# Kernel tuning notes

Measured on AMD Instinct MI355X. Metric: run time of the kernel, lower is better.

The kernel has to match this reference:

```python
import jax, jax.numpy as jnp
import numpy as np

VOCAB_SIZE = 148
START_IDX = 1
LATENT = 32
HID = 256
NUM_LAYERS = 2
B = 8192
T = 50


def setup_inputs() -> dict:
    key = jax.random.key(0)
    ks = jax.random.split(key, 20)
    s = 0.05
    inp = {
        "z": jax.random.normal(ks[0], (B, LATENT), jnp.float32),
        "target_tokens": jax.random.randint(ks[1], (B, T), 0, VOCAB_SIZE),
        "emb": jax.random.normal(ks[2], (VOCAB_SIZE, HID), jnp.float32) * s,
        "W_lat": jax.random.normal(ks[3], (HID * NUM_LAYERS, LATENT), jnp.float32) * s,
        "b_lat": jnp.zeros((HID * NUM_LAYERS,), jnp.float32),
        "W_ih0": jax.random.normal(ks[4], (3 * HID, HID), jnp.float32) * s,
        "W_hh0": jax.random.normal(ks[5], (3 * HID, HID), jnp.float32) * s,
        "b_ih0": jnp.zeros((3 * HID,), jnp.float32),
        "b_hh0": jnp.zeros((3 * HID,), jnp.float32),
        "W_ih1": jax.random.normal(ks[6], (3 * HID, HID), jnp.float32) * s,
        "W_hh1": jax.random.normal(ks[7], (3 * HID, HID), jnp.float32) * s,
        "b_ih1": jnp.zeros((3 * HID,), jnp.float32),
        "b_hh1": jnp.zeros((3 * HID,), jnp.float32),
        "W1": jax.random.normal(ks[8], (HID, HID), jnp.float32) * s,
        "b1": jnp.zeros((HID,), jnp.float32),
        "W2": jax.random.normal(ks[9], (VOCAB_SIZE, HID), jnp.float32) * s,
        "b2": jnp.zeros((VOCAB_SIZE,), jnp.float32),
    }
    # padding_idx=0 row of embedding is zero in torch
    inp["emb"] = inp["emb"].at[0].set(0.0)
    return inp


def _gru_cell(x, h, W_ih, W_hh, b_ih, b_hh):
    # PyTorch GRUCell math
    gi = x @ W_ih.T + b_ih          # [B, 3H]
    gh = h @ W_hh.T + b_hh          # [B, 3H]
    i_r, i_z, i_n = jnp.split(gi, 3, axis=-1)
    h_r, h_z, h_n = jnp.split(gh, 3, axis=-1)
    r = jax.nn.sigmoid(i_r + h_r)
    zg = jax.nn.sigmoid(i_z + h_z)
    n = jnp.tanh(i_n + r * h_n)
    return (1.0 - zg) * n + zg * h


def reference(z, target_tokens, emb, W_lat, b_lat,
              W_ih0, W_hh0, b_ih0, b_hh0,
              W_ih1, W_hh1, b_ih1, b_hh1,
              W1, b1, W2, b2):
    batch = z.shape[0]
    # init hidden: (B, L*H) -> (L, B, H)
    h = (z @ W_lat.T + b_lat).reshape(batch, NUM_LAYERS, HID).transpose(1, 0, 2)
    # teacher forcing ratio 1.0: inputs = [START, tgt[:,1], ..., tgt[:,T-2]]
    start = jnp.full((batch, 1), START_IDX, dtype=target_tokens.dtype)
    tokens_in = jnp.concatenate([start, target_tokens[:, 1:T - 1]], axis=1)  # [B, T-1]
    x = emb[tokens_in]                       # [B, T-1, H]
    xs = x.transpose(1, 0, 2)                # [T-1, B, H]

    def step(carry, x_t):
        h0, h1 = carry
        h0n = _gru_cell(x_t, h0, W_ih0, W_hh0, b_ih0, b_hh0)
        h1n = _gru_cell(h0n, h1, W_ih1, W_hh1, b_ih1, b_hh1)
        return (h0n, h1n), h1n

    _, ys = jax.lax.scan(step, (h[0], h[1]), xs)   # ys: [T-1, B, H]
    y = ys.transpose(1, 0, 2)                      # [B, T-1, H]
    hdd = jax.nn.relu(jnp.einsum('bth,oh->bto', y, W1) + b1)
    logits = jnp.einsum('bth,vh->btv', hdd, W2) + b2   # [B, T-1, V]
    generated = target_tokens[:, 1:]                   # pure teacher forcing
    return logits, generated
```

## Files before the change

### kernel.cpp

```cpp
#include <hip/hip_runtime.h>
#include <hip/hip_bf16.h>
#include <math.h>


#define BATCH 8192
#define TTOT 50
#define TS 49
#define HID 256
#define N3 768
#define VOCAB 148
#define START_TOK 1
#define HPAD 264

typedef short bf16x8 __attribute__((ext_vector_type(8)));
typedef float f32x4 __attribute__((ext_vector_type(4)));

constexpr size_t OFF_Y    = 0;
constexpr size_t OFF_WH0B = OFF_Y + 205520896;
constexpr size_t OFF_WI1B = OFF_WH0B + 393216;
constexpr size_t OFF_WH1B = OFF_WI1B + 393216;
constexpr size_t OFF_W1B  = OFF_WH1B + 393216;
constexpr size_t OFF_W2B  = OFF_W1B + 131072;
constexpr size_t OFF_TAB  = OFF_W2B + 81920;
constexpr size_t OFF_TABN = OFF_TAB + 303104;
constexpr size_t OFF_H0F  = OFF_TAB + 454656;
constexpr size_t OFF_H1F  = OFF_H0F + 8388608;

__device__ __forceinline__ short f2b(float f) {
    union { float f; unsigned int u; } v; v.f = f;
    unsigned int u = v.u;
    return (short)((u + 0x7FFFu + ((u >> 16) & 1u)) >> 16);
}
__device__ __forceinline__ float sigm(float x) {
    return 1.f / (1.f + __expf(-x));
}
__device__ __forceinline__ float tanh_(float x) {
    x = fmaxf(x, -15.f);
    float e = __expf(-2.f * x);
    return (1.f - e) / (1.f + e);
}

__global__ __launch_bounds__(256) void convert_w(
    const float* __restrict__ Wh0, const float* __restrict__ Wi1, const float* __restrict__ Wh1,
    const float* __restrict__ W1, const float* __restrict__ W2,
    short* __restrict__ Wh0b, short* __restrict__ Wi1b, short* __restrict__ Wh1b,
    short* __restrict__ W1b, short* __restrict__ W2b)
{
    int tid = blockIdx.x * 256 + threadIdx.x;
    const int WSZ = N3 * HID;
    const float* S; short* D; int n; bool pad148 = false;
    if (tid < WSZ) { S = Wh0; D = Wh0b; n = tid; }
    else if (tid < 2 * WSZ) { S = Wi1; D = Wi1b; n = tid - WSZ; }
    else if (tid < 3 * WSZ) { S = Wh1; D = Wh1b; n = tid - 2 * WSZ; }
    else if (tid < 3 * WSZ + 65536) { S = W1; D = W1b; n = tid - 3 * WSZ; }
    else if (tid < 3 * WSZ + 65536 + 40960) { S = W2; D = W2b; n = tid - 3 * WSZ - 65536; pad148 = true; }
    else return;
    int e = n & 7, lane = (n >> 3) & 63, kc = (n >> 9) & 7, nt = n >> 12;
    int row = nt * 16 + (lane & 15);
    int k = kc * 32 + (lane >> 4) * 8 + e;
    float v = (pad148 && row >= VOCAB) ? 0.f : S[row * HID + k];
    D[n] = f2b(v);
}

__global__ __launch_bounds__(256) void build_tab2(
    const float* __restrict__ emb, const float* __restrict__ Wih0,
    const float* __restrict__ bih0, const float* __restrict__ bhh0,
    float* __restrict__ tab_rz, float* __restrict__ tab_n)
{
    int o = blockIdx.x * 256 + threadIdx.x;
    if (o >= VOCAB * N3) return;
    int v = o / N3, cc = o - v * N3;
    int g = cc >> 8, c = cc & 255;
    const float* er = emb + v * HID;
    const float* wr = Wih0 + cc * HID;
    float s = bih0[cc];
    #pragma unroll 8
    for (int k = 0; k < HID; ++k) s += er[k] * wr[k];
    if (g == 0)      tab_rz[(((v << 8) + c) << 1) + 0] = s + bhh0[c];
    else if (g == 1) tab_rz[(((v << 8) + c) << 1) + 1] = s + bhh0[256 + c];
    else             tab_n[(v << 8) + c] = s;
}

__global__ __launch_bounds__(256) void init_h(
    const float* __restrict__ z, const float* __restrict__ Wl, const float* __restrict__ bl,
    float* __restrict__ h0f, float* __restrict__ h1f)
{
    int tid = blockIdx.x * 256 + threadIdx.x;
    int b = tid >> 9, o = tid & 511;
    const float* zr = z + b * 32;
    const float* wr = Wl + o * 32;
    float s = bl[o];
    #pragma unroll
    for (int k = 0; k < 32; ++k) s += zr[k] * wr[k];
    if (o < HID) h0f[b * HID + o] = s;
    else         h1f[b * HID + o - HID] = s;
}

__global__ __launch_bounds__(512) __attribute__((amdgpu_waves_per_eu(4)))
void gru_persistent(
    const int* __restrict__ toks,
    const float* __restrict__ tab_rz, const float* __restrict__ tab_n,
    const short* __restrict__ Wh0, const short* __restrict__ Wi1, const short* __restrict__ Wh1,
    const float* __restrict__ bhh0, const float* __restrict__ bih1, const float* __restrict__ bhh1,
    const float* __restrict__ h0f, const float* __restrict__ h1f,
    short* __restrict__ Yb)
{
    __shared__ short h0L[2][16 * HPAD];
    __shared__ short h1L[2][16 * HPAD];
    __shared__ int tokL[16 * TTOT];

    const int tid = threadIdx.x;
    const int wave = tid >> 6, lane = tid & 63, quad = lane >> 4, l15 = lane & 15;
    const int rowbase = blockIdx.x * 16;

    {
        int row = tid >> 5, col = (tid & 31) * 8;
        const float* s0 = h0f + (size_t)(rowbase + row) * HID + col;
        const float* s1 = h1f + (size_t)(rowbase + row) * HID + col;
        short t0[8], t1[8];
        #pragma unroll
        for (int j = 0; j < 8; ++j) { t0[j] = f2b(s0[j]); t1[j] = f2b(s1[j]); }
        *(bf16x8*)&h0L[0][row * HPAD + col] = *(bf16x8*)t0;
        *(bf16x8*)&h1L[0][row * HPAD + col] = *(bf16x8*)t1;
    }
    for (int idx = tid; idx < 16 * TTOT; idx += 512) {
        int row = idx / TTOT, tt = idx - row * TTOT;
        tokL[idx] = (tt == 0) ? START_TOK : toks[(size_t)(rowbase + row) * TTOT + tt];
    }

    int colc[2]; colc[0] = wave * 32 + l15; colc[1] = colc[0] + 16;
    float h0r[2][4], h1r[2][4];
    #pragma unroll
    for (int c = 0; c < 2; ++c)
        #pragma unroll
        for (int r_ = 0; r_ < 4; ++r_) {
            int row = rowbase + quad * 4 + r_;
            h0r[c][r_] = h0f[(size_t)row * HID + colc[c]];
            h1r[c][r_] = h1f[(size_t)row * HID + colc[c]];
        }

    float bn0[2], brr[2], brz[2], bni[2], bnh[2];
    #pragma unroll
    for (int c = 0; c < 2; ++c) {
        int col = colc[c];
        bn0[c] = bhh0[512 + col];
        brr[c] = bih1[col] + bhh1[col];
        brz[c] = bih1[256 + col] + bhh1[256 + col];
        bni[c] = bih1[512 + col];
        bnh[c] = bhh1[512 + col];
    }

    int woff[6];
    #pragma unroll
    for (int g = 0; g < 3; ++g)
        #pragma unroll
        for (int c = 0; c < 2; ++c)
            woff[g * 2 + c] = ((g * 16 + wave * 2 + c) << 12) + lane * 8;

    const int a0base = l15 * HPAD + quad * 8;
    const int hwbase = (quad * 4) * HPAD + colc[0];
    int tokrow[4];
    #pragma unroll
    for (int r_ = 0; r_ < 4; ++r_) tokrow[r_] = (quad * 4 + r_) * TTOT;
    short* yptr = Yb + ((((size_t)blockIdx.x << 3) + wave) << 9) + lane * 8;

    int rb = 0, wb = 1;
    __syncthreads();

    for (int t = 0; t < TS; ++t) {
        f32x4 acc0[6] = {};
        #pragma unroll 1
        for (int kc = 0; kc < 8; ++kc) {
            bf16x8 a0 = *(const bf16x8*)&h0L[rb][a0base + kc * 32];
            #pragma unroll
            for (int j = 0; j < 6; ++j) {
                bf16x8 b0 = *(const bf16x8*)(Wh0 + woff[j] + kc * 512);
                acc0[j] = __builtin_amdgcn_mfma_f32_16x16x32_bf16(a0, b0, acc0[j], 0, 0, 0);
            }
        }
        #pragma unroll
        for (int r_ = 0; r_ < 4; ++r_) {
            int tok = tokL[tokrow[r_] + t];
            const float2 rz0 = *(const float2*)(tab_rz + (tok << 9) + (colc[0] << 1));
            const float2 rz1 = *(const float2*)(tab_rz + (tok << 9) + (colc[1] << 1));
            float in0 = tab_n[(tok << 8) + colc[0]];
            float in1 = tab_n[(tok << 8) + colc[1]];
            {
                float r = sigm(acc0[0][r_] + rz0.x);
                float z = sigm(acc0[2][r_] + rz0.y);
                float n = tanh_(in0 + r * (acc0[4][r_] + bn0[0]));
                h0r[0][r_] = n + z * (h0r[0][r_] - n);
            }
            {
                float r = sigm(acc0[1][r_] + rz1.x);
                float z = sigm(acc0[3][r_] + rz1.y);
                float n = tanh_(in1 + r * (acc0[5][r_] + bn0[1]));
                h0r[1][r_] = n + z * (h0r[1][r_] - n);
            }
        }
        #pragma unroll
        for (int r_ = 0; r_ < 4; ++r_) {
            unsigned u;
            asm("v_cvt_pk_bf16_f32 %0, %1, %2" : "=v"(u) : "v"(h0r[0][r_]), "v"(h0r[1][r_]));
            int ro = hwbase + r_ * HPAD;
            h0L[wb][ro]      = (short)u;
            h0L[wb][ro + 16] = (short)(u >> 16);
        }
        __syncthreads();

        f32x4 accrz[4] = {}, acchn[2] = {}, accgn[2] = {};
        #pragma unroll 1
        for (int kc = 0; kc < 8; ++kc) {
            bf16x8 a1 = *(const bf16x8*)&h1L[rb][a0base + kc * 32];
            bf16x8 an = *(const bf16x8*)&h0L[wb][a0base + kc * 32];
            #pragma unroll
            for (int j = 0; j < 6; ++j) {
                bf16x8 b1 = *(const bf16x8*)(Wh1 + woff[j] + kc * 512);
                if (j < 4) accrz[j] = __builtin_amdgcn_mfma_f32_16x16x32_bf16(a1, b1, accrz[j], 0, 0, 0);
                else       acchn[j - 4] = __builtin_amdgcn_mfma_f32_16x16x32_bf16(a1, b1, acchn[j - 4], 0, 0, 0);
            }
            #pragma unroll
            for (int j = 0; j < 6; ++j) {
                bf16x8 b = *(const bf16x8*)(Wi1 + woff[j] + kc * 512);
                if (j < 4) accrz[j] = __builtin_amdgcn_mfma_f32_16x16x32_bf16(an, b, accrz[j], 0, 0, 0);
                else       accgn[j - 4] = __builtin_amdgcn_mfma_f32_16x16x32_bf16(an, b, accgn[j - 4], 0, 0, 0);
            }
        }
        #pragma unroll
        for (int c = 0; c < 2; ++c)
            #pragma unroll
            for (int r_ = 0; r_ < 4; ++r_) {
                float r = sigm(accrz[c][r_] + brr[c]);
                float z = sigm(accrz[2 + c][r_] + brz[c]);
                float n = tanh_(accgn[c][r_] + bni[c] + r * (acchn[c][r_] + bnh[c]));
                h1r[c][r_] = n + z * (h1r[c][r_] - n);
            }
        #pragma unroll
        for (int r_ = 0; r_ < 4; ++r_) {
            unsigned u;
            asm("v_cvt_pk_bf16_f32 %0, %1, %2" : "=v"(u) : "v"(h1r[0][r_]), "v"(h1r[1][r_]));
            int ro = hwbase + r_ * HPAD;
            h1L[wb][ro]      = (short)u;
            h1L[wb][ro + 16] = (short)(u >> 16);
        }
        __syncthreads();

        *(bf16x8*)yptr = *(const bf16x8*)&h1L[wb][a0base + wave * 32];
        yptr += (size_t)512 * 8 * 512;

        rb ^= 1; wb ^= 1;
    }
}

__global__ __launch_bounds__(256) void head_kernel(
    const short* __restrict__ YP, const short* __restrict__ W1P, const float* __restrict__ b1,
    const short* __restrict__ W2P, const float* __restrict__ b2, float* __restrict__ out)
{
    __shared__ short hddL[64 * HPAD];
    int wave = threadIdx.x >> 6;
    int lane = threadIdx.x & 63;
    int quad = lane >> 4;
    int l15  = lane & 15;
    int rbase = blockIdx.x * 64;
    int tt = rbase >> 13;
    int mb = (rbase & 8191) >> 4;

    {
        const short* ybase = YP + ((size_t)tt * 512 + mb) * 4096 + lane * 8;
        const short* wbase = W1P + (size_t)(wave * 4) * 4096 + lane * 8;
        f32x4 acc[4][4] = {};
        #pragma unroll 2
        for (int kc = 0; kc < 8; ++kc) {
            bf16x8 a[4], bfr[4];
            #pragma unroll
            for (int i = 0; i < 4; ++i) a[i] = *(const bf16x8*)(ybase + (size_t)i * 4096 + kc * 512);
            #pragma unroll
            for (int j = 0; j < 4; ++j) bfr[j] = *(const bf16x8*)(wbase + (size_t)j * 4096 + kc * 512);
            #pragma unroll
            for (int i = 0; i < 4; ++i)
                #pragma unroll
                for (int j = 0; j < 4; ++j)
                    acc[i][j] = __builtin_amdgcn_mfma_f32_16x16x32_bf16(a[i], bfr[j], acc[i][j], 0, 0, 0);
        }
        #pragma unroll
        for (int i = 0; i < 4; ++i)
            #pragma unroll
            for (int j = 0; j < 4; ++j)
                #pragma unroll
                for (int r = 0; r < 4; ++r) {
                    int rl = i * 16 + quad * 4 + r;
                    int c  = wave * 64 + j * 16 + l15;
                    float v = acc[i][j][r] + b1[c];
                    hddL[rl * HPAD + c] = f2b(fmaxf(v, 0.f));
                }
    }
    __syncthreads();
    for (int s = wave * 5; s < wave * 5 + 5; ++s) {
        int ct = s >> 1, rh = s & 1;
        const short* w2b = W2P + (size_t)ct * 4096 + lane * 8;
        f32x4 acc2[2] = {};
        #pragma unroll 2
        for (int kc = 0; kc < 8; ++kc) {
            bf16x8 bfr = *(const bf16x8*)(w2b + kc * 512);
            #pragma unroll
            for (int it = 0; it < 2; ++it) {
                bf16x8 a = *(const bf16x8*)&hddL[(rh * 32 + it * 16 + l15) * HPAD + kc * 32 + quad * 8];
                acc2[it] = __builtin_amdgcn_mfma_f32_16x16x32_bf16(a, bfr, acc2[it], 0, 0, 0);
            }
        }
        int col = ct * 16 + l15;
        if (col < VOCAB) {
            #pragma unroll
            for (int it = 0; it < 2; ++it)
                #pragma unroll
                for (int r = 0; r < 4; ++r) {
                    int rl = rh * 32 + it * 16 + quad * 4 + r;
                    int gr = rbase + rl;
                    int t2 = gr >> 13;
                    int bb = gr & 8191;
                    out[((size_t)bb * TS + t2) * VOCAB + col] = acc2[it][r] + b2[col];
                }
        }
    }
}

__global__ __launch_bounds__(256) void gen_copy(const int* __restrict__ toks, float* __restrict__ out2)
{
    int tid = blockIdx.x * 256 + threadIdx.x;
    if (tid < BATCH * TS) {
        int b = tid / TS, j = tid - b * TS;
        out2[tid] = (float)toks[b * TTOT + j + 1];
    }
}

extern "C" void kernel_launch(void* const* d_in, const int* in_sizes, int n_in,
                              void* d_out, int out_size, void* d_ws, size_t ws_size,
                              hipStream_t stream) {
    const float* z     = (const float*)d_in[0];
    const int*   toks  = (const int*)d_in[1];
    const float* emb   = (const float*)d_in[2];
    const float* W_lat = (const float*)d_in[3];
    const float* b_lat = (const float*)d_in[4];
    const float* W_ih0 = (const float*)d_in[5];
    const float* W_hh0 = (const float*)d_in[6];
    const float* b_ih0 = (const float*)d_in[7];
    const float* b_hh0 = (const float*)d_in[8];
    const float* W_ih1 = (const float*)d_in[9];
    const float* W_hh1 = (const float*)d_in[10];
    const float* b_ih1 = (const float*)d_in[11];
    const float* b_hh1 = (const float*)d_in[12];
    const float* W1    = (const float*)d_in[13];
    const float* b1    = (const float*)d_in[14];
    const float* W2    = (const float*)d_in[15];
    const float* b2    = (const float*)d_in[16];

    char* w = (char*)d_ws;
    short* Yb    = (short*)(w + OFF_Y);
    short* Wh0b  = (short*)(w + OFF_WH0B);
    short* Wi1b  = (short*)(w + OFF_WI1B);
    short* Wh1b  = (short*)(w + OFF_WH1B);
    short* W1b   = (short*)(w + OFF_W1B);
    short* W2b   = (short*)(w + OFF_W2B);
    float* tabrz = (float*)(w + OFF_TAB);
    float* tabn  = (float*)(w + OFF_TABN);
    float* h0f   = (float*)(w + OFF_H0F);
    float* h1f   = (float*)(w + OFF_H1F);

    float* out_logits = (float*)d_out;
    float* out_gen    = out_logits + (size_t)BATCH * TS * VOCAB;

    convert_w<<<2720, 256, 0, stream>>>(W_hh0, W_ih1, W_hh1, W1, W2,
                                        Wh0b, Wi1b, Wh1b, W1b, W2b);
    build_tab2<<<(VOCAB * N3 + 255) / 256, 256, 0, stream>>>(emb, W_ih0, b_ih0, b_hh0, tabrz, tabn);
    init_h<<<(BATCH * 512) / 256, 256, 0, stream>>>(z, W_lat, b_lat, h0f, h1f);
    gen_copy<<<(BATCH * TS + 255) / 256, 256, 0, stream>>>(toks, out_gen);

    gru_persistent<<<512, 512, 0, stream>>>(toks, tabrz, tabn, Wh0b, Wi1b, Wh1b,
                                            b_hh0, b_ih1, b_hh1, h0f, h1f, Yb);

    head_kernel<<<(BATCH * TS) / 64, 256, 0, stream>>>(Yb, W1b, b1, W2b, b2, out_logits);
}
```

Baseline: 1.723 ms.

## Retile GRU kernel to 32 rows per block with 16 waves, reusing weight loads

The persistent GRU kernel now handles 32 batch rows per block using 1024 threads. Each wave owns 16 hidden columns for two 16-row M tiles instead of 32 columns for one tile, so every weight fragment loaded from global memory feeds two MFMAs. This is meant to halve per-block weight traffic and the grid is halved to 256 blocks. In exchange each CU gets fewer blocks and there are more waves per barrier, and the 1024-thread launch bound combined with waves_per_eu(4) may constrain register allocation.

```diff
diff --git a/kernel.cpp b/kernel.cpp
--- a/kernel.cpp
+++ b/kernel.cpp
@@ -96,7 +96,7 @@
     else         h1f[b * HID + o - HID] = s;
 }
 
-__global__ __launch_bounds__(512) __attribute__((amdgpu_waves_per_eu(4)))
+__global__ __launch_bounds__(1024) __attribute__((amdgpu_waves_per_eu(4)))
 void gru_persistent(
     const int* __restrict__ toks,
     const float* __restrict__ tab_rz, const float* __restrict__ tab_n,
@@ -105,13 +105,13 @@
     const float* __restrict__ h0f, const float* __restrict__ h1f,
     short* __restrict__ Yb)
 {
-    __shared__ short h0L[2][16 * HPAD];
-    __shared__ short h1L[2][16 * HPAD];
-    __shared__ int tokL[16 * TTOT];
+    __shared__ short h0L[2][32 * HPAD];
+    __shared__ short h1L[2][32 * HPAD];
+    __shared__ int tokL[32 * TTOT];
 
     const int tid = threadIdx.x;
     const int wave = tid >> 6, lane = tid & 63, quad = lane >> 4, l15 = lane & 15;
-    const int rowbase = blockIdx.x * 16;
+    const int rowbase = blockIdx.x * 32;
 
     {
         int row = tid >> 5, col = (tid & 31) * 8;
@@ -123,129 +123,126 @@
         *(bf16x8*)&h0L[0][row * HPAD + col] = *(bf16x8*)t0;
         *(bf16x8*)&h1L[0][row * HPAD + col] = *(bf16x8*)t1;
     }
-    for (int idx = tid; idx < 16 * TTOT; idx += 512) {
+    for (int idx = tid; idx < 32 * TTOT; idx += 1024) {
         int row = idx / TTOT, tt = idx - row * TTOT;
         tokL[idx] = (tt == 0) ? START_TOK : toks[(size_t)(rowbase + row) * TTOT + tt];
     }
 
-    int colc[2]; colc[0] = wave * 32 + l15; colc[1] = colc[0] + 16;
+    const int colc = wave * 16 + l15;
     float h0r[2][4], h1r[2][4];
     #pragma unroll
-    for (int c = 0; c < 2; ++c)
+    for (int i = 0; i < 2; ++i)
         #pragma unroll
         for (int r_ = 0; r_ < 4; ++r_) {
-            int row = rowbase + quad * 4 + r_;
-            h0r[c][r_] = h0f[(size_t)row * HID + colc[c]];
-            h1r[c][r_] = h1f[(size_t)row * HID + colc[c]];
-        }
-
-    float bn0[2], brr[2], brz[2], bni[2], bnh[2];
-    #pragma unroll
-    for (int c = 0; c < 2; ++c) {
-        int col = colc[c];
-        bn0[c] = bhh0[512 + col];
-        brr[c] = bih1[col] + bhh1[col];
-        brz[c] = bih1[256 + col] + bhh1[256 + col];
-        bni[c] = bih1[512 + col];
-        bnh[c] = bhh1[512 + col];
-    }
-
-    int woff[6];
+            int row = rowbase + 16 * i + quad * 4 + r_;
+            h0r[i][r_] = h0f[(size_t)row * HID + colc];
+            h1r[i][r_] = h1f[(size_t)row * HID + colc];
+        }
+
+    const float bn0 = bhh0[512 + colc];
+    const float brr = bih1[colc] + bhh1[colc];
+    const float brz = bih1[256 + colc] + bhh1[256 + colc];
+    const float bni = bih1[512 + colc];
+    const float bnh = bhh1[512 + colc];
+
+    int woff[3];
     #pragma unroll
     for (int g = 0; g < 3; ++g)
-        #pragma unroll
-        for (int c = 0; c < 2; ++c)
-            woff[g * 2 + c] = ((g * 16 + wave * 2 + c) << 12) + lane * 8;
-
-    const int a0base = l15 * HPAD + quad * 8;
-    const int hwbase = (quad * 4) * HPAD + colc[0];
-    int tokrow[4];
-    #pragma unroll
-    for (int r_ = 0; r_ < 4; ++r_) tokrow[r_] = (quad * 4 + r_) * TTOT;
-    short* yptr = Yb + ((((size_t)blockIdx.x << 3) + wave) << 9) + lane * 8;
+        woff[g] = ((g * 16 + wave) << 12) + lane * 8;
+
+    const int abase0 = l15 * HPAD + quad * 8;
+    const int abase1 = (16 + l15) * HPAD + quad * 8;
+    const int hwbase = (quad * 4) * HPAD + colc;
+    const int ybase  = ((wave >> 3) * 16 + l15) * HPAD + (wave & 7) * 32 + quad * 8;
+    short* yptr = Yb + ((((size_t)(blockIdx.x * 2 + (wave >> 3))) * 8 + (wave & 7)) << 9) + lane * 8;
 
     int rb = 0, wb = 1;
     __syncthreads();
 
     for (int t = 0; t < TS; ++t) {
-        f32x4 acc0[6] = {};
+        f32x4 acc0[2][3] = {};
         #pragma unroll 1
         for (int kc = 0; kc < 8; ++kc) {
-            bf16x8 a0 = *(const bf16x8*)&h0L[rb][a0base + kc * 32];
-            #pragma unroll
-            for (int j = 0; j < 6; ++j) {
-                bf16x8 b0 = *(const bf16x8*)(Wh0 + woff[j] + kc * 512);
-                acc0[j] = __builtin_amdgcn_mfma_f32_16x16x32_bf16(a0, b0, acc0[j], 0, 0, 0);
-            }
-        }
-        #pragma unroll
-        for (int r_ = 0; r_ < 4; ++r_) {
-            int tok = tokL[tokrow[r_] + t];
-            const float2 rz0 = *(const float2*)(tab_rz + (tok << 9) + (colc[0] << 1));
-            const float2 rz1 = *(const float2*)(tab_rz + (tok << 9) + (colc[1] << 1));
-            float in0 = tab_n[(tok << 8) + colc[0]];
-            float in1 = tab_n[(tok << 8) + colc[1]];
-            {
-                float r = sigm(acc0[0][r_] + rz0.x);
-                float z = sigm(acc0[2][r_] + rz0.y);
-                float n = tanh_(in0 + r * (acc0[4][r_] + bn0[0]));
-                h0r[0][r_] = n + z * (h0r[0][r_] - n);
-            }
-            {
-                float r = sigm(acc0[1][r_] + rz1.x);
-                float z = sigm(acc0[3][r_] + rz1.y);
-                float n = tanh_(in1 + r * (acc0[5][r_] + bn0[1]));
-                h0r[1][r_] = n + z * (h0r[1][r_] - n);
-            }
-        }
+            bf16x8 a0[2];
+            a0[0] = *(const bf16x8*)&h0L[rb][abase0 + kc * 32];
+            a0[1] = *(const bf16x8*)&h0L[rb][abase1 + kc * 32];
+            #pragma unroll
+            for (int g = 0; g < 3; ++g) {
+                bf16x8 b = *(const bf16x8*)(Wh0 + woff[g] + kc * 512);
+                #pragma unroll
+                for (int i = 0; i < 2; ++i)
+                    acc0[i][g] = __builtin_amdgcn_mfma_f32_16x16x32_bf16(a0[i], b, acc0[i][g], 0, 0, 0);
+            }
+        }
+        #pragma unroll
+        for (int i = 0; i < 2; ++i)
+            #pragma unroll
+            for (int r_ = 0; r_ < 4; ++r_) {
+                int tok = tokL[(16 * i + quad * 4 + r_) * TTOT + t];
+                const float2 rz = *(const float2*)(tab_rz + (tok << 9) + (colc << 1));
+                float inn = tab_n[(tok << 8) + colc];
+                float r = sigm(acc0[i][0][r_] + rz.x);
+                float z = sigm(acc0[i][1][r_] + rz.y);
+                float n = tanh_(inn + r * (acc0[i][2][r_] + bn0));
+                h0r[i][r_] = n + z * (h0r[i][r_] - n);
+            }
         #pragma unroll
         for (int r_ = 0; r_ < 4; ++r_) {
             unsigned u;
             asm("v_cvt_pk_bf16_f32 %0, %1, %2" : "=v"(u) : "v"(h0r[0][r_]), "v"(h0r[1][r_]));
             int ro = hwbase + r_ * HPAD;
-            h0L[wb][ro]      = (short)u;
-            h0L[wb][ro + 16] = (short)(u >> 16);
+            h0L[wb][ro]             = (short)u;
+            h0L[wb][ro + 16 * HPAD] = (short)(u >> 16);
         }
         __syncthreads();
 
-        f32x4 accrz[4] = {}, acchn[2] = {}, accgn[2] = {};
+        f32x4 accrz[2][2] = {}, acchn[2] = {}, accgn[2] = {};
         #pragma unroll 1
         for (int kc = 0; kc < 8; ++kc) {
-            bf16x8 a1 = *(const bf16x8*)&h1L[rb][a0base + kc * 32];
-            bf16x8 an = *(const bf16x8*)&h0L[wb][a0base + kc * 32];
-            #pragma unroll
-            for (int j = 0; j < 6; ++j) {
-                bf16x8 b1 = *(const bf16x8*)(Wh1 + woff[j] + kc * 512);
-                if (j < 4) accrz[j] = __builtin_amdgcn_mfma_f32_16x16x32_bf16(a1, b1, accrz[j], 0, 0, 0);
-                else       acchn[j - 4] = __builtin_amdgcn_mfma_f32_16x16x32_bf16(a1, b1, acchn[j - 4], 0, 0, 0);
-            }
-            #pragma unroll
-            for (int j = 0; j < 6; ++j) {
-                bf16x8 b = *(const bf16x8*)(Wi1 + woff[j] + kc * 512);
-                if (j < 4) accrz[j] = __builtin_amdgcn_mfma_f32_16x16x32_bf16(an, b, accrz[j], 0, 0, 0);
-                else       accgn[j - 4] = __builtin_amdgcn_mfma_f32_16x16x32_bf16(an, b, accgn[j - 4], 0, 0, 0);
-            }
-        }
-        #pragma unroll
-        for (int c = 0; c < 2; ++c)
+            bf16x8 a1[2], an[2];
+            a1[0] = *(const bf16x8*)&h1L[rb][abase0 + kc * 32];
+            a1[1] = *(const bf16x8*)&h1L[rb][abase1 + kc * 32];
+            an[0] = *(const bf16x8*)&h0L[wb][abase0 + kc * 32];
+            an[1] = *(const bf16x8*)&h0L[wb][abase1 + kc * 32];
+            #pragma unroll
+            for (int g = 0; g < 3; ++g) {
+                bf16x8 b1 = *(const bf16x8*)(Wh1 + woff[g] + kc * 512);
+                #pragma unroll
+                for (int i = 0; i < 2; ++i) {
+                    if (g < 2) accrz[i][g] = __builtin_amdgcn_mfma_f32_16x16x32_bf16(a1[i], b1, accrz[i][g], 0, 0, 0);
+                    else       acchn[i] = __builtin_amdgcn_mfma_f32_16x16x32_bf16(a1[i], b1, acchn[i], 0, 0, 0);
+                }
+            }
+            #pragma unroll
+            for (int g = 0; g < 3; ++g) {
+                bf16x8 b = *(const bf16x8*)(Wi1 + woff[g] + kc * 512);
+                #pragma unroll
+                for (int i = 0; i < 2; ++i) {
+                    if (g < 2) accrz[i][g] = __builtin_amdgcn_mfma_f32_16x16x32_bf16(an[i], b, accrz[i][g], 0, 0, 0);
+                    else       accgn[i] = __builtin_amdgcn_mfma_f32_16x16x32_bf16(an[i], b, accgn[i], 0, 0, 0);
+                }
+            }
+        }
+        #pragma unroll
+        for (int i = 0; i < 2; ++i)
             #pragma unroll
             for (int r_ = 0; r_ < 4; ++r_) {
-                float r = sigm(accrz[c][r_] + brr[c]);
-                float z = sigm(accrz[2 + c][r_] + brz[c]);
-                float n = tanh_(accgn[c][r_] + bni[c] + r * (acchn[c][r_] + bnh[c]));
-                h1r[c][r_] = n + z * (h1r[c][r_] - n);
+                float r = sigm(accrz[i][0][r_] + brr);
+                float z = sigm(accrz[i][1][r_] + brz);
+                float n = tanh_(accgn[i][r_] + bni + r * (acchn[i][r_] + bnh));
+                h1r[i][r_] = n + z * (h1r[i][r_] - n);
             }
         #pragma unroll
         for (int r_ = 0; r_ < 4; ++r_) {
             unsigned u;
             asm("v_cvt_pk_bf16_f32 %0, %1, %2" : "=v"(u) : "v"(h1r[0][r_]), "v"(h1r[1][r_]));
             int ro = hwbase + r_ * HPAD;
-            h1L[wb][ro]      = (short)u;
-            h1L[wb][ro + 16] = (short)(u >> 16);
+            h1L[wb][ro]             = (short)u;
+            h1L[wb][ro + 16 * HPAD] = (short)(u >> 16);
         }
         __syncthreads();
 
-        *(bf16x8*)yptr = *(const bf16x8*)&h1L[wb][a0base + wave * 32];
+        *(bf16x8*)yptr = *(const bf16x8*)&h1L[wb][ybase];
         yptr += (size_t)512 * 8 * 512;
 
         rb ^= 1; wb ^= 1;
@@ -375,8 +372,8 @@
     init_h<<<(BATCH * 512) / 256, 256, 0, stream>>>(z, W_lat, b_lat, h0f, h1f);
     gen_copy<<<(BATCH * TS + 255) / 256, 256, 0, stream>>>(toks, out_gen);
 
-    gru_persistent<<<512, 512, 0, stream>>>(toks, tabrz, tabn, Wh0b, Wi1b, Wh1b,
-                                            b_hh0, b_ih1, b_hh1, h0f, h1f, Yb);
+    gru_persistent<<<256, 1024, 0, stream>>>(toks, tabrz, tabn, Wh0b, Wi1b, Wh1b,
+                                             b_hh0, b_ih1, b_hh1, h0f, h1f, Yb);
 
     head_kernel<<<(BATCH * TS) / 64, 256, 0, stream>>>(Yb, W1b, b1, W2b, b2, out_logits);
 }
```

After: 1.404 ms. 1.23x faster.
